# Kernel optimization log

Hardware: AMD Instinct MI355X
Metric: run time of the kernel (lower is better)

## Reference

```python
import jax, jax.numpy as jnp
import numpy as np

B, D, H = 8, 512, 8
HD = D // H            # 64 head dim
NS, NT = 8192, 4096    # search / template points
ATTN_EPS = 1e-6
LN_EPS = 1e-5


def layer_norm(x, g, b):
    m = jnp.mean(x, axis=-1, keepdims=True)
    v = jnp.mean((x - m) ** 2, axis=-1, keepdims=True)
    return (x - m) * jax.lax.rsqrt(v + LN_EPS) * g + b


def setup_inputs() -> dict:
    key = jax.random.key(0)
    ks = jax.random.split(key, 20)
    s = 0.02
    return {
        "search_feat": jax.random.normal(ks[0], (B, D, NS), jnp.float32),
        "search_xyz": jax.random.uniform(ks[1], (B, NS, 3), jnp.float32),
        "template_feat": jax.random.normal(ks[2], (B, D, NT), jnp.float32),
        "template_xyz": jax.random.uniform(ks[3], (B, NT, 3), jnp.float32),
        "pos_w1": jax.random.normal(ks[4], (3, D), jnp.float32) * s,
        "pos_b1": jnp.zeros((D,), jnp.float32),
        "pos_w2": jax.random.normal(ks[5], (D, D), jnp.float32) * s,
        "pos_b2": jnp.zeros((D,), jnp.float32),
        "wq": jax.random.normal(ks[6], (D, D), jnp.float32) * s,
        "wk": jax.random.normal(ks[7], (D, D), jnp.float32) * s,
        "wv": jax.random.normal(ks[8], (D, D), jnp.float32) * s,
        "w_merge": jax.random.normal(ks[9], (D, D), jnp.float32) * s,
        "mlp_w1": jax.random.normal(ks[10], (2 * D, 2 * D), jnp.float32) * s,
        "mlp_w2": jax.random.normal(ks[11], (2 * D, D), jnp.float32) * s,
        "ln1_g": jnp.ones((D,), jnp.float32),
        "ln1_b": jnp.zeros((D,), jnp.float32),
        "ln2_g": jnp.ones((D,), jnp.float32),
        "ln2_b": jnp.zeros((D,), jnp.float32),
    }


def reference(search_feat, search_xyz, template_feat, template_xyz,
              pos_w1, pos_b1, pos_w2, pos_b2, wq, wk, wv, w_merge,
              mlp_w1, mlp_w2, ln1_g, ln1_b, ln2_g, ln2_b):
    bs = search_feat.shape[0]
    sf = jnp.transpose(search_feat, (0, 2, 1))    # [B, Ns, D]
    tf = jnp.transpose(template_feat, (0, 2, 1))  # [B, Nt, D]

    # positional MLP on template coordinates
    pos = jax.nn.relu(template_xyz @ pos_w1 + pos_b1) @ pos_w2 + pos_b2
    tf_pos = tf + pos

    q = (sf @ wq).reshape(bs, NS, H, HD)
    k = (tf @ wk).reshape(bs, NT, H, HD)
    v = (tf_pos @ wv).reshape(bs, NT, H, HD)

    # LoFTR-style linear attention: phi(x) = elu(x) + 1
    Q = jax.nn.elu(q) + 1.0
    K = jax.nn.elu(k) + 1.0
    v_len = v.shape[1]
    v_n = v / v_len
    KV = jnp.einsum("bshd,bshv->bhdv", K, v_n)                 # [B,H,d,d]
    Z = 1.0 / (jnp.einsum("blhd,bhd->blh", Q, K.sum(axis=1)) + ATTN_EPS)
    msg = jnp.einsum("blhd,bhdv->blhv", Q, KV) * Z[..., None] * v_len

    msg = msg.reshape(bs, NS, H * HD) @ w_merge
    msg = layer_norm(msg, ln1_g, ln1_b)
    cat = jnp.concatenate([sf, msg], axis=2)                    # [B,Ns,2D]
    msg = jax.nn.relu(cat @ mlp_w1) @ mlp_w2
    msg = layer_norm(msg, ln2_g, ln2_b)
    return jnp.transpose(sf + msg, (0, 2, 1))                   # [B,D,Ns]
```

## Files before the change

kernel.cpp:

```cpp
#include <hip/hip_runtime.h>
#include <stdint.h>
#include <stddef.h>


using ushort_t = unsigned short;
using short8 = __attribute__((ext_vector_type(8))) short;
using f32x4  = __attribute__((ext_vector_type(4))) float;

#define DEVI __device__ __forceinline__

DEVI float b2f(unsigned short u) {
    unsigned v = ((unsigned)u) << 16;
    return __builtin_bit_cast(float, v);
}
DEVI unsigned short f2b(float x) {
    unsigned u = __builtin_bit_cast(unsigned, x);
    u += 0x7FFFu + ((u >> 16) & 1u);
    return (unsigned short)(u >> 16);
}
DEVI void gload16(const void* g, void* l) {
    __builtin_amdgcn_global_load_lds(
        (const __attribute__((address_space(1))) unsigned*)g,
        (__attribute__((address_space(3))) unsigned*)l, 16, 0, 0);
}

template <int EPI>
__global__ __launch_bounds__(512, 2)
void gemm_bf16(const ushort_t* __restrict__ A0, const ushort_t* __restrict__ A1,
               const ushort_t* __restrict__ Wt, ushort_t* __restrict__ C,
               const float* __restrict__ bias, const ushort_t* __restrict__ addm,
               int N, int K, int K0, int lda0, int lda1, int nn)
{
    __shared__ ushort_t As[2][256 * 64];
    __shared__ ushort_t Bs[2][256 * 64];
    const int tid = threadIdx.x;
    const int cpx = gridDim.x >> 3;
    const int lid = (blockIdx.x & 7) * cpx + (blockIdx.x >> 3);
    const int m0 = (lid / nn) * 256;
    const int n0 = (lid % nn) * 256;
    const int w = tid >> 6, l = tid & 63;
    const int wm = (w >> 2) * 128;
    const int wn = (w & 3) * 64;
    const int lr = l & 15, lg = l >> 4;
    const int srow = tid >> 3;
    const int sck  = (tid & 7) ^ (srow & 7);
    const int nk = K / 64;

    f32x4 acc[8][4] = {};

    auto stageA = [&](int kt, int buf) {
        const int kb = kt * 64;
        const ushort_t* p; int ld;
        if (kb < K0) { p = A0 + (size_t)m0 * lda0 + kb; ld = lda0; }
        else         { p = A1 + (size_t)m0 * lda1 + (kb - K0); ld = lda1; }
        p += (size_t)srow * ld + sck * 8;
#pragma unroll
        for (int j = 0; j < 4; j++)
            gload16(p + (size_t)(j * 64) * ld,
                    (void*)(&As[buf][j * 4096] + tid * 8));
    };
    auto stageB = [&](int kt, int buf) {
        const ushort_t* p = Wt + (size_t)(n0 + srow) * K + kt * 64 + sck * 8;
#pragma unroll
        for (int j = 0; j < 4; j++)
            gload16(p + (size_t)(j * 64) * K,
                    (void*)(&Bs[buf][j * 4096] + tid * 8));
    };

    stageA(0, 0); stageB(0, 0);
    asm volatile("s_waitcnt vmcnt(0)" ::: "memory");
    asm volatile("s_barrier" ::: "memory");

    for (int t = 0; t < nk; ++t) {
        const int cur = t & 1;
        const bool pre = (t + 1) < nk;
        short8 afr[4], bfr[4];

        auto ldA = [&](int mh, int ks) {
#pragma unroll
            for (int mf = 0; mf < 4; mf++) {
                const int r = wm + mh * 64 + mf * 16 + lr;
                afr[mf] = *(const short8*)&As[cur][r * 64 + ((ks * 4 + lg) ^ (r & 7)) * 8];
            }
        };
        auto ldB = [&](int ks) {
#pragma unroll
            for (int nf = 0; nf < 4; nf++) {
                const int r = wn + nf * 16 + lr;
                bfr[nf] = *(const short8*)&Bs[cur][r * 64 + ((ks * 4 + lg) ^ (r & 7)) * 8];
            }
        };
        auto mm = [&](int mh) {
            __builtin_amdgcn_s_setprio(1);
#pragma unroll
            for (int mf = 0; mf < 4; mf++)
#pragma unroll
                for (int nf = 0; nf < 4; nf++)
                    acc[mh * 4 + mf][nf] = __builtin_amdgcn_mfma_f32_16x16x32_bf16(
                        afr[mf], bfr[nf], acc[mh * 4 + mf][nf], 0, 0, 0);
            __builtin_amdgcn_s_setprio(0);
        };

        ldB(0); ldA(0, 0);
        if (pre) stageA(t + 1, cur ^ 1);
        asm volatile("s_barrier" ::: "memory");
        mm(0);
        asm volatile("s_barrier" ::: "memory");
        ldA(1, 0);
        if (pre) stageB(t + 1, cur ^ 1);
        asm volatile("s_barrier" ::: "memory");
        mm(1);
        asm volatile("s_barrier" ::: "memory");
        ldB(1); ldA(0, 1);
        asm volatile("s_barrier" ::: "memory");
        mm(0);
        asm volatile("s_barrier" ::: "memory");
        ldA(1, 1);
        asm volatile("s_waitcnt vmcnt(0)" ::: "memory");
        asm volatile("s_barrier" ::: "memory");
        mm(1);
        asm volatile("s_barrier" ::: "memory");
    }

#pragma unroll
    for (int mi = 0; mi < 8; mi++) {
        const int mh = mi >> 2, mf = mi & 3;
#pragma unroll
        for (int i = 0; i < 4; i++) {
            const int m = m0 + wm + mh * 64 + mf * 16 + lg * 4 + i;
#pragma unroll
            for (int nf = 0; nf < 4; nf++) {
                const int n = n0 + wn + nf * 16 + lr;
                float x = acc[mi][nf][i];
                if constexpr (EPI == 1) { x = x > 0.f ? x + 1.f : __expf(x); }
                if constexpr (EPI == 2) { x += bias[n] + b2f(addm[(size_t)m * N + n]); }
                if constexpr (EPI == 3) { x = fmaxf(x, 0.f); }
                C[(size_t)m * N + n] = f2b(x);
            }
        }
    }
}

__global__ __launch_bounds__(256)
void transpose_f32_bf16(const float* __restrict__ in, ushort_t* __restrict__ out,
                        int R, int Cc)
{
    __shared__ float tile[64][65];
    const int t = threadIdx.x;
    const int c0 = blockIdx.x * 64, r0 = blockIdx.y * 64;
    const size_t bo = (size_t)blockIdx.z * (size_t)R * (size_t)Cc;
    const float* src = in + bo;
    ushort_t* dst = out + bo;
#pragma unroll
    for (int i = 0; i < 4; i++) {
        const int r = (t >> 4) + i * 16;
        const int c = (t & 15) * 4;
        const float4 v = *(const float4*)&src[(size_t)(r0 + r) * Cc + c0 + c];
        tile[r][c + 0] = v.x; tile[r][c + 1] = v.y;
        tile[r][c + 2] = v.z; tile[r][c + 3] = v.w;
    }
    __syncthreads();
#pragma unroll
    for (int i = 0; i < 2; i++) {
        const int c = (t >> 3) + i * 32;
        const int rs = (t & 7) * 8;
        short8 o;
#pragma unroll
        for (int j = 0; j < 8; j++) o[j] = (short)f2b(tile[rs + j][c]);
        *(short8*)&dst[(size_t)(c0 + c) * R + r0 + rs] = o;
    }
}

__global__ __launch_bounds__(256)
void pos_mlp1(const float* __restrict__ xyz, const float* __restrict__ w1,
              const float* __restrict__ b1, ushort_t* __restrict__ P1)
{
    const int t = threadIdx.x;
    const int m = blockIdx.x * 4 + (t >> 6);
    const int n0 = (t & 63) * 8;
    const float x = xyz[m * 3 + 0], y = xyz[m * 3 + 1], z = xyz[m * 3 + 2];
    short8 o;
#pragma unroll
    for (int j = 0; j < 8; j++) {
        const int n = n0 + j;
        float v = x * w1[n] + y * w1[512 + n] + z * w1[1024 + n] + b1[n];
        o[j] = (short)f2b(fmaxf(v, 0.f));
    }
    *(short8*)&P1[(size_t)m * 512 + n0] = o;
}

__global__ __launch_bounds__(256)
void kv_partial(const ushort_t* __restrict__ Kp, const ushort_t* __restrict__ V,
                float* __restrict__ KVp, float* __restrict__ Ksp)
{
    __shared__ ushort_t Ks[256 * 64];
    __shared__ ushort_t Vs[256 * 64];
    const int t = threadIdx.x;
    const int sp = blockIdx.x, h = blockIdx.y, b = blockIdx.z;
    const int d0 = t >> 2, e0 = (t & 3) * 16;
    const int srow = t >> 3, scol = (t & 7) * 8;
    float acc[16] = {};
    float ksum = 0.f;
    for (int c = 0; c < 4; c++) {
        if (c) __syncthreads();
        const size_t sbase = (size_t)b * 4096 + sp * 1024 + c * 256;
#pragma unroll
        for (int i = 0; i < 8; i++) {
            const size_t go = (sbase + i * 32 + srow) * 512 + h * 64 + scol;
            gload16(Kp + go, (void*)(&Ks[i * 2048] + t * 8));
            gload16(V + go, (void*)(&Vs[i * 2048] + t * 8));
        }
        __syncthreads();
        for (int s = 0; s < 256; s++) {
            const float k = b2f(Ks[s * 64 + d0]);
            if ((t & 3) == 0) ksum += k;
            const short8 v0 = *(const short8*)&Vs[s * 64 + e0];
            const short8 v1 = *(const short8*)&Vs[s * 64 + e0 + 8];
#pragma unroll
            for (int j = 0; j < 8; j++) {
                acc[j]     += k * b2f((unsigned short)v0[j]);
                acc[8 + j] += k * b2f((unsigned short)v1[j]);
            }
        }
    }
    const int bh = b * 8 + h;
    float* kvo = KVp + (((size_t)sp * 64 + bh) * 64 + d0) * 64 + e0;
#pragma unroll
    for (int j = 0; j < 16; j++) kvo[j] = acc[j];
    if ((t & 3) == 0) Ksp[((size_t)sp * 64 + bh) * 64 + d0] = ksum;
}

__global__ __launch_bounds__(256)
void kv_finalize(const float* __restrict__ KVp, const float* __restrict__ Ksp,
                 ushort_t* __restrict__ KVt)
{
    const int bh = blockIdx.x, t = threadIdx.x;
    ushort_t* o = KVt + (size_t)bh * 5120;
#pragma unroll
    for (int i = 0; i < 16; i++) {
        const int idx = i * 256 + t;
        const int e = idx >> 6, d = idx & 63;
        float s = 0.f;
#pragma unroll
        for (int sp = 0; sp < 4; sp++)
            s += KVp[(((size_t)sp * 64 + bh) * 64 + d) * 64 + e];
        o[idx] = f2b(s);
    }
    if (t < 64) {
        float s = 0.f;
#pragma unroll
        for (int sp = 0; sp < 4; sp++) s += Ksp[((size_t)sp * 64 + bh) * 64 + t];
        o[4096 + t] = f2b(s);
    }
    for (int idx = 4160 + t; idx < 5120; idx += 256) o[idx] = 0;
}

__global__ __launch_bounds__(256, 2)
void attn_apply(const ushort_t* __restrict__ Qp, const ushort_t* __restrict__ KVt,
                ushort_t* __restrict__ msg1)
{
    __shared__ ushort_t As[256 * 64];
    __shared__ ushort_t Bs[80 * 64];
    const int t = threadIdx.x;
    const int ch = blockIdx.x, h = blockIdx.y, b = blockIdx.z;
    const int w = t >> 6, l = t & 63;
    const int lr = l & 15, lg = l >> 4;
    const int row0 = ch * 256;
    const int srow = t >> 3;
    const int sc = ((t & 7) ^ (srow & 7)) * 8;
    const ushort_t* kv = KVt + (size_t)(b * 8 + h) * 5120;
#pragma unroll
    for (int i = 0; i < 2; i++)
        gload16(kv + (size_t)(i * 32 + srow) * 64 + sc,
                (void*)(&Bs[i * 2048] + t * 8));
    if (t < 128)
        gload16(kv + (size_t)(64 + srow) * 64 + sc,
                (void*)(&Bs[4096] + t * 8));
    const ushort_t* qb = Qp + ((size_t)b * 8192 + row0) * 512 + h * 64;
#pragma unroll
    for (int i = 0; i < 8; i++)
        gload16(qb + (size_t)(i * 32 + srow) * 512 + sc,
                (void*)(&As[i * 2048] + t * 8));
    __syncthreads();
    f32x4 acc[4][5] = {};
    const int wr = w * 64;
#pragma unroll
    for (int ks = 0; ks < 2; ks++) {
        const int kswz = ((ks * 4 + lg) ^ (lr & 7)) * 8;
        short8 a[4], bb[5];
#pragma unroll
        for (int mf = 0; mf < 4; mf++)
            a[mf] = *(const short8*)&As[(wr + mf * 16 + lr) * 64 + kswz];
#pragma unroll
        for (int nf = 0; nf < 5; nf++)
            bb[nf] = *(const short8*)&Bs[(nf * 16 + lr) * 64 + kswz];
#pragma unroll
        for (int mf = 0; mf < 4; mf++)
#pragma unroll
            for (int nf = 0; nf < 5; nf++)
                acc[mf][nf] = __builtin_amdgcn_mfma_f32_16x16x32_bf16(
                    a[mf], bb[nf], acc[mf][nf], 0, 0, 0);
    }
#pragma unroll
    for (int mf = 0; mf < 4; mf++) {
#pragma unroll
        for (int i = 0; i < 4; i++) {
            const int m = row0 + wr + mf * 16 + lg * 4 + i;
            const float zden = __shfl(acc[mf][4][i], (l & 48));
            const float z = 1.f / (zden + 1e-6f);
#pragma unroll
            for (int nf = 0; nf < 4; nf++) {
                const int e = nf * 16 + lr;
                msg1[((size_t)b * 8192 + m) * 512 + h * 64 + e] =
                    f2b(acc[mf][nf][i] * z);
            }
        }
    }
}

__global__ __launch_bounds__(256)
void layer_norm_k(ushort_t* __restrict__ X, const float* __restrict__ g,
                  const float* __restrict__ bta)
{
    const int t = threadIdx.x;
    const int row = blockIdx.x * 4 + (t >> 6);
    const int l = t & 63;
    ushort_t* x = X + (size_t)row * 512;
    const short8 v = *(const short8*)&x[l * 8];
    float f[8];
    float s = 0.f;
#pragma unroll
    for (int j = 0; j < 8; j++) { f[j] = b2f((unsigned short)v[j]); s += f[j]; }
#pragma unroll
    for (int o = 32; o > 0; o >>= 1) s += __shfl_xor(s, o);
    const float mean = s * (1.f / 512.f);
    float vs = 0.f;
#pragma unroll
    for (int j = 0; j < 8; j++) { const float d = f[j] - mean; vs += d * d; }
#pragma unroll
    for (int o = 32; o > 0; o >>= 1) vs += __shfl_xor(vs, o);
    const float rstd = rsqrtf(vs * (1.f / 512.f) + 1e-5f);
    short8 ov;
#pragma unroll
    for (int j = 0; j < 8; j++) {
        const int c = l * 8 + j;
        ov[j] = (short)f2b((f[j] - mean) * rstd * g[c] + bta[c]);
    }
    *(short8*)&x[l * 8] = ov;
}

__global__ __launch_bounds__(256)
void ln2_final(const ushort_t* __restrict__ outp, const ushort_t* __restrict__ sfT,
               const float* __restrict__ g, const float* __restrict__ bta,
               float* __restrict__ out)
{
    __shared__ ushort_t tile[64][514];
    const int t = threadIdx.x;
    const int ns0 = blockIdx.x * 64, b = blockIdx.y;
    const int w = t >> 6, l = t & 63;
#pragma unroll
    for (int rr = 0; rr < 16; rr++) {
        const int r = w * 16 + rr;
        const size_t grow = (size_t)b * 8192 + ns0 + r;
        const short8 v = *(const short8*)&outp[grow * 512 + l * 8];
        float f[8];
        float s = 0.f;
#pragma unroll
        for (int j = 0; j < 8; j++) { f[j] = b2f((unsigned short)v[j]); s += f[j]; }
#pragma unroll
        for (int o = 32; o > 0; o >>= 1) s += __shfl_xor(s, o);
        const float mean = s * (1.f / 512.f);
        float vs = 0.f;
#pragma unroll
        for (int j = 0; j < 8; j++) { const float d = f[j] - mean; vs += d * d; }
#pragma unroll
        for (int o = 32; o > 0; o >>= 1) vs += __shfl_xor(vs, o);
        const float rstd = rsqrtf(vs * (1.f / 512.f) + 1e-5f);
        const short8 sv = *(const short8*)&sfT[grow * 512 + l * 8];
        short8 ov;
#pragma unroll
        for (int j = 0; j < 8; j++) {
            const int c = l * 8 + j;
            ov[j] = (short)f2b(b2f((unsigned short)sv[j]) +
                               (f[j] - mean) * rstd * g[c] + bta[c]);
        }
        *(short8*)&tile[r][l * 8] = ov;
    }
    __syncthreads();
#pragma unroll
    for (int i = 0; i < 32; i++) {
        const int d = (t >> 4) + i * 16;
        const int nss = (t & 15) * 4;
        float4 o;
        o.x = b2f(tile[nss + 0][d]);
        o.y = b2f(tile[nss + 1][d]);
        o.z = b2f(tile[nss + 2][d]);
        o.w = b2f(tile[nss + 3][d]);
        *(float4*)&out[((size_t)b * 512 + d) * 8192 + ns0 + nss] = o;
    }
}

extern "C" void kernel_launch(void* const* d_in, const int* in_sizes, int n_in,
                              void* d_out, int out_size, void* d_ws, size_t ws_size,
                              hipStream_t stream)
{
    (void)in_sizes; (void)n_in; (void)out_size; (void)ws_size;
    const float* search_feat   = (const float*)d_in[0];
    const float* template_feat = (const float*)d_in[2];
    const float* template_xyz  = (const float*)d_in[3];
    const float* pos_w1  = (const float*)d_in[4];
    const float* pos_b1  = (const float*)d_in[5];
    const float* pos_w2  = (const float*)d_in[6];
    const float* pos_b2  = (const float*)d_in[7];
    const float* wq      = (const float*)d_in[8];
    const float* wk      = (const float*)d_in[9];
    const float* wv      = (const float*)d_in[10];
    const float* w_merge = (const float*)d_in[11];
    const float* mlp_w1  = (const float*)d_in[12];
    const float* mlp_w2  = (const float*)d_in[13];
    const float* ln1_g   = (const float*)d_in[14];
    const float* ln1_b   = (const float*)d_in[15];
    const float* ln2_g   = (const float*)d_in[16];
    const float* ln2_b   = (const float*)d_in[17];
    float* out = (float*)d_out;

    char* ws = (char*)d_ws;
    ushort_t* sfT    = (ushort_t*)(ws + 0);
    ushort_t* Qp     = (ushort_t*)(ws + 67108864);
    ushort_t* tfT    = (ushort_t*)(ws + 134217728);
    ushort_t* Kp     = (ushort_t*)(ws + 167772160);
    ushort_t* msg2   = (ushort_t*)(ws + 134217728);
    ushort_t* P1     = (ushort_t*)(ws + 201326592);
    ushort_t* Vv     = (ushort_t*)(ws + 201326592);
    ushort_t* tfpos  = (ushort_t*)(ws + 234881024);
    ushort_t* msg1   = (ushort_t*)(ws + 268435456);
    ushort_t* hidden = (ushort_t*)(ws + 201326592);
    ushort_t* outp   = Qp;
    ushort_t* wqT  = (ushort_t*)(ws + 335544320);
    ushort_t* wkT  = (ushort_t*)(ws + 336068608);
    ushort_t* wvT  = (ushort_t*)(ws + 336592896);
    ushort_t* wmT  = (ushort_t*)(ws + 337117184);
    ushort_t* pw2T = (ushort_t*)(ws + 337641472);
    ushort_t* w1T  = (ushort_t*)(ws + 338165760);
    ushort_t* w2T  = (ushort_t*)(ws + 340262912);
    float*    KVp  = (float*)(ws + 341311488);
    float*    Ksp  = (float*)(ws + 345505792);
    ushort_t* KVt  = (ushort_t*)(ws + 345571328);

    transpose_f32_bf16<<<dim3(128, 8, 8), 256, 0, stream>>>(search_feat, sfT, 512, 8192);
    transpose_f32_bf16<<<dim3(64, 8, 8), 256, 0, stream>>>(template_feat, tfT, 512, 4096);
    transpose_f32_bf16<<<dim3(8, 8, 1), 256, 0, stream>>>(wq, wqT, 512, 512);
    transpose_f32_bf16<<<dim3(8, 8, 1), 256, 0, stream>>>(wk, wkT, 512, 512);
    transpose_f32_bf16<<<dim3(8, 8, 1), 256, 0, stream>>>(wv, wvT, 512, 512);
    transpose_f32_bf16<<<dim3(8, 8, 1), 256, 0, stream>>>(w_merge, wmT, 512, 512);
    transpose_f32_bf16<<<dim3(8, 8, 1), 256, 0, stream>>>(pos_w2, pw2T, 512, 512);
    transpose_f32_bf16<<<dim3(16, 16, 1), 256, 0, stream>>>(mlp_w1, w1T, 1024, 1024);
    transpose_f32_bf16<<<dim3(8, 16, 1), 256, 0, stream>>>(mlp_w2, w2T, 1024, 512);

    gemm_bf16<1><<<dim3(512), 512, 0, stream>>>(sfT, nullptr, wqT, Qp,
                                                nullptr, nullptr, 512, 512, 512, 512, 0, 2);
    gemm_bf16<1><<<dim3(256), 512, 0, stream>>>(tfT, nullptr, wkT, Kp,
                                                nullptr, nullptr, 512, 512, 512, 512, 0, 2);
    pos_mlp1<<<dim3(8192), 256, 0, stream>>>(template_xyz, pos_w1, pos_b1, P1);
    gemm_bf16<2><<<dim3(256), 512, 0, stream>>>(P1, nullptr, pw2T, tfpos,
                                                pos_b2, tfT, 512, 512, 512, 512, 0, 2);
    gemm_bf16<0><<<dim3(256), 512, 0, stream>>>(tfpos, nullptr, wvT, Vv,
                                                nullptr, nullptr, 512, 512, 512, 512, 0, 2);
    kv_partial<<<dim3(4, 8, 8), 256, 0, stream>>>(Kp, Vv, KVp, Ksp);
    kv_finalize<<<dim3(64), 256, 0, stream>>>(KVp, Ksp, KVt);
    attn_apply<<<dim3(32, 8, 8), 256, 0, stream>>>(Qp, KVt, msg1);
    gemm_bf16<0><<<dim3(512), 512, 0, stream>>>(msg1, nullptr, wmT, msg2,
                                                nullptr, nullptr, 512, 512, 512, 512, 0, 2);
    layer_norm_k<<<dim3(16384), 256, 0, stream>>>(msg2, ln1_g, ln1_b);
    gemm_bf16<3><<<dim3(1024), 512, 0, stream>>>(sfT, msg2, w1T, hidden,
                                                 nullptr, nullptr, 1024, 1024, 512, 512, 512, 4);
    gemm_bf16<0><<<dim3(512), 512, 0, stream>>>(hidden, nullptr, w2T, outp,
                                                nullptr, nullptr, 512, 1024, 1024, 1024, 0, 2);
    ln2_final<<<dim3(128, 8), 256, 0, stream>>>(outp, sfT, ln2_g, ln2_b, out);
}
```

Baseline: 741.3 us.

## Software-pipeline GEMM LDS fragment loads and cut per-iteration barriers to one

Reworks the bf16 MFMA GEMM main loop so LDS fragment reads are double-buffered in registers (aP/aQ/aR, b0/b1). Each fragment set is loaded one MFMA block ahead of its use, and the eight barriers per k-tile drop to a single barrier after the global prefetch completes. The accumulators are split into two 4x4 halves, and the epilogue is adjusted to match. The aim is to overlap LDS reads with MFMA work and remove synchronization stalls, at the cost of more live fragment registers and possible occupancy or spill pressure.

Result: faster. 707.1 us (-4.6%).

```diff
diff --git a/kernel.cpp b/kernel.cpp
--- a/kernel.cpp
+++ b/kernel.cpp
@@ -46,7 +46,8 @@
     const int sck  = (tid & 7) ^ (srow & 7);
     const int nk = K / 64;
 
-    f32x4 acc[8][4] = {};
+    f32x4 accA[4][4] = {};
+    f32x4 accB[4][4] = {};
 
     auto stageA = [&](int kt, int buf) {
         const int kb = kt * 64;
@@ -67,75 +68,79 @@
                     (void*)(&Bs[buf][j * 4096] + tid * 8));
     };
 
+    short8 aP[4], aQ[4], aR[4], b0[4], b1[4];
+
+    auto ldA = [&](short8 (&dst)[4], int mh, int ks, int cb) {
+#pragma unroll
+        for (int mf = 0; mf < 4; mf++) {
+            const int r = wm + mh * 64 + mf * 16 + lr;
+            dst[mf] = *(const short8*)&As[cb][r * 64 + ((ks * 4 + lg) ^ (r & 7)) * 8];
+        }
+    };
+    auto ldB = [&](short8 (&dst)[4], int ks, int cb) {
+#pragma unroll
+        for (int nf = 0; nf < 4; nf++) {
+            const int r = wn + nf * 16 + lr;
+            dst[nf] = *(const short8*)&Bs[cb][r * 64 + ((ks * 4 + lg) ^ (r & 7)) * 8];
+        }
+    };
+    auto MM = [&](f32x4 (&ac)[4][4], short8 (&af)[4], short8 (&bf)[4]) {
+        __builtin_amdgcn_s_setprio(1);
+#pragma unroll
+        for (int mf = 0; mf < 4; mf++)
+#pragma unroll
+            for (int nf = 0; nf < 4; nf++)
+                ac[mf][nf] = __builtin_amdgcn_mfma_f32_16x16x32_bf16(
+                    af[mf], bf[nf], ac[mf][nf], 0, 0, 0);
+        __builtin_amdgcn_s_setprio(0);
+    };
+
     stageA(0, 0); stageB(0, 0);
     asm volatile("s_waitcnt vmcnt(0)" ::: "memory");
-    asm volatile("s_barrier" ::: "memory");
+    __builtin_amdgcn_s_barrier();
+    ldA(aP, 0, 0, 0); ldB(b0, 0, 0);
 
     for (int t = 0; t < nk; ++t) {
         const int cur = t & 1;
         const bool pre = (t + 1) < nk;
-        short8 afr[4], bfr[4];
-
-        auto ldA = [&](int mh, int ks) {
-#pragma unroll
-            for (int mf = 0; mf < 4; mf++) {
-                const int r = wm + mh * 64 + mf * 16 + lr;
-                afr[mf] = *(const short8*)&As[cur][r * 64 + ((ks * 4 + lg) ^ (r & 7)) * 8];
-            }
-        };
-        auto ldB = [&](int ks) {
-#pragma unroll
-            for (int nf = 0; nf < 4; nf++) {
-                const int r = wn + nf * 16 + lr;
-                bfr[nf] = *(const short8*)&Bs[cur][r * 64 + ((ks * 4 + lg) ^ (r & 7)) * 8];
-            }
-        };
-        auto mm = [&](int mh) {
-            __builtin_amdgcn_s_setprio(1);
-#pragma unroll
-            for (int mf = 0; mf < 4; mf++)
-#pragma unroll
-                for (int nf = 0; nf < 4; nf++)
-                    acc[mh * 4 + mf][nf] = __builtin_amdgcn_mfma_f32_16x16x32_bf16(
-                        afr[mf], bfr[nf], acc[mh * 4 + mf][nf], 0, 0, 0);
-            __builtin_amdgcn_s_setprio(0);
-        };
-
-        ldB(0); ldA(0, 0);
+        ldA(aQ, 1, 0, cur); ldB(b1, 1, cur);
         if (pre) stageA(t + 1, cur ^ 1);
-        asm volatile("s_barrier" ::: "memory");
-        mm(0);
-        asm volatile("s_barrier" ::: "memory");
-        ldA(1, 0);
+        MM(accA, aP, b0);
+        ldA(aR, 0, 1, cur);
         if (pre) stageB(t + 1, cur ^ 1);
-        asm volatile("s_barrier" ::: "memory");
-        mm(1);
-        asm volatile("s_barrier" ::: "memory");
-        ldB(1); ldA(0, 1);
-        asm volatile("s_barrier" ::: "memory");
-        mm(0);
-        asm volatile("s_barrier" ::: "memory");
-        ldA(1, 1);
-        asm volatile("s_waitcnt vmcnt(0)" ::: "memory");
-        asm volatile("s_barrier" ::: "memory");
-        mm(1);
-        asm volatile("s_barrier" ::: "memory");
-    }
-
-#pragma unroll
-    for (int mi = 0; mi < 8; mi++) {
-        const int mh = mi >> 2, mf = mi & 3;
+        MM(accB, aQ, b0);
+        ldA(aP, 1, 1, cur);
+        MM(accA, aR, b1);
+        MM(accB, aP, b1);
+        if (pre) {
+            asm volatile("s_waitcnt vmcnt(0)" ::: "memory");
+            __builtin_amdgcn_s_barrier();
+            ldA(aP, 0, 0, cur ^ 1); ldB(b0, 0, cur ^ 1);
+        }
+    }
+
+#pragma unroll
+    for (int mf = 0; mf < 4; mf++) {
 #pragma unroll
         for (int i = 0; i < 4; i++) {
-            const int m = m0 + wm + mh * 64 + mf * 16 + lg * 4 + i;
+            const int mA = m0 + wm + mf * 16 + lg * 4 + i;
+            const int mB = mA + 64;
 #pragma unroll
             for (int nf = 0; nf < 4; nf++) {
                 const int n = n0 + wn + nf * 16 + lr;
-                float x = acc[mi][nf][i];
-                if constexpr (EPI == 1) { x = x > 0.f ? x + 1.f : __expf(x); }
-                if constexpr (EPI == 2) { x += bias[n] + b2f(addm[(size_t)m * N + n]); }
-                if constexpr (EPI == 3) { x = fmaxf(x, 0.f); }
-                C[(size_t)m * N + n] = f2b(x);
+                float x = accA[mf][nf][i];
+                float y = accB[mf][nf][i];
+                if constexpr (EPI == 1) {
+                    x = x > 0.f ? x + 1.f : __expf(x);
+                    y = y > 0.f ? y + 1.f : __expf(y);
+                }
+                if constexpr (EPI == 2) {
+                    x += bias[n] + b2f(addm[(size_t)mA * N + n]);
+                    y += bias[n] + b2f(addm[(size_t)mB * N + n]);
+                }
+                if constexpr (EPI == 3) { x = fmaxf(x, 0.f); y = fmaxf(y, 0.f); }
+                C[(size_t)mA * N + n] = f2b(x);
+                C[(size_t)mB * N + n] = f2b(y);
             }
         }
     }
```

## Restructure GEMM main loop into 4-buffer BK=32 pipeline with prefetch distance 2

Applied to the files above, without the earlier changes.

Replaces the double-buffered BK=64 GEMM loop, which had many intra-iteration barriers, with a 4-slot ring of BK=32 tiles. Loads run two stages ahead and each iteration ends with a single vmcnt wait and barrier. The LDS footprint is the same, and the swizzle is changed to suit 32-wide rows. The aim is to overlap global loads with MFMA and cut barrier count, at the cost of a shorter K step per barrier and possible new LDS bank conflicts from the narrower swizzle.

Result: slower. 825.4 us (+11.4%).

```diff
diff --git a/kernel.cpp b/kernel.cpp
--- a/kernel.cpp
+++ b/kernel.cpp
@@ -31,8 +31,8 @@
                const float* __restrict__ bias, const ushort_t* __restrict__ addm,
                int N, int K, int K0, int lda0, int lda1, int nn)
 {
-    __shared__ ushort_t As[2][256 * 64];
-    __shared__ ushort_t Bs[2][256 * 64];
+    __shared__ ushort_t As[4][256 * 32];
+    __shared__ ushort_t Bs[4][256 * 32];
     const int tid = threadIdx.x;
     const int cpx = gridDim.x >> 3;
     const int lid = (blockIdx.x & 7) * cpx + (blockIdx.x >> 3);
@@ -42,96 +42,77 @@
     const int wm = (w >> 2) * 128;
     const int wn = (w & 3) * 64;
     const int lr = l & 15, lg = l >> 4;
-    const int srow = tid >> 3;
-    const int sck  = (tid & 7) ^ (srow & 7);
-    const int nk = K / 64;
+    const int srow = tid >> 2;
+    const int sck  = (tid & 3) ^ ((srow >> 1) & 3);
+    const int nk = K / 32;
 
     f32x4 acc[8][4] = {};
 
     auto stageA = [&](int kt, int buf) {
-        const int kb = kt * 64;
+        const int kb = kt * 32;
         const ushort_t* p; int ld;
         if (kb < K0) { p = A0 + (size_t)m0 * lda0 + kb; ld = lda0; }
         else         { p = A1 + (size_t)m0 * lda1 + (kb - K0); ld = lda1; }
         p += (size_t)srow * ld + sck * 8;
 #pragma unroll
-        for (int j = 0; j < 4; j++)
-            gload16(p + (size_t)(j * 64) * ld,
+        for (int j = 0; j < 2; j++)
+            gload16(p + (size_t)(j * 128) * ld,
                     (void*)(&As[buf][j * 4096] + tid * 8));
     };
     auto stageB = [&](int kt, int buf) {
-        const ushort_t* p = Wt + (size_t)(n0 + srow) * K + kt * 64 + sck * 8;
-#pragma unroll
-        for (int j = 0; j < 4; j++)
-            gload16(p + (size_t)(j * 64) * K,
+        const ushort_t* p = Wt + (size_t)(n0 + srow) * K + kt * 32 + sck * 8;
+#pragma unroll
+        for (int j = 0; j < 2; j++)
+            gload16(p + (size_t)(j * 128) * K,
                     (void*)(&Bs[buf][j * 4096] + tid * 8));
     };
 
     stageA(0, 0); stageB(0, 0);
-    asm volatile("s_waitcnt vmcnt(0)" ::: "memory");
-    asm volatile("s_barrier" ::: "memory");
+    stageA(1, 1); stageB(1, 1);
+    asm volatile("s_waitcnt vmcnt(4)" ::: "memory");
+    __builtin_amdgcn_s_barrier();
 
     for (int t = 0; t < nk; ++t) {
-        const int cur = t & 1;
-        const bool pre = (t + 1) < nk;
-        short8 afr[4], bfr[4];
-
-        auto ldA = [&](int mh, int ks) {
-#pragma unroll
-            for (int mf = 0; mf < 4; mf++) {
-                const int r = wm + mh * 64 + mf * 16 + lr;
-                afr[mf] = *(const short8*)&As[cur][r * 64 + ((ks * 4 + lg) ^ (r & 7)) * 8];
-            }
-        };
-        auto ldB = [&](int ks) {
-#pragma unroll
-            for (int nf = 0; nf < 4; nf++) {
-                const int r = wn + nf * 16 + lr;
-                bfr[nf] = *(const short8*)&Bs[cur][r * 64 + ((ks * 4 + lg) ^ (r & 7)) * 8];
-            }
-        };
-        auto mm = [&](int mh) {
-            __builtin_amdgcn_s_setprio(1);
-#pragma unroll
-            for (int mf = 0; mf < 4; mf++)
-#pragma unroll
-                for (int nf = 0; nf < 4; nf++)
-                    acc[mh * 4 + mf][nf] = __builtin_amdgcn_mfma_f32_16x16x32_bf16(
-                        afr[mf], bfr[nf], acc[mh * 4 + mf][nf], 0, 0, 0);
-            __builtin_amdgcn_s_setprio(0);
-        };
-
-        ldB(0); ldA(0, 0);
-        if (pre) stageA(t + 1, cur ^ 1);
-        asm volatile("s_barrier" ::: "memory");
-        mm(0);
-        asm volatile("s_barrier" ::: "memory");
-        ldA(1, 0);
-        if (pre) stageB(t + 1, cur ^ 1);
-        asm volatile("s_barrier" ::: "memory");
-        mm(1);
-        asm volatile("s_barrier" ::: "memory");
-        ldB(1); ldA(0, 1);
-        asm volatile("s_barrier" ::: "memory");
-        mm(0);
-        asm volatile("s_barrier" ::: "memory");
-        ldA(1, 1);
-        asm volatile("s_waitcnt vmcnt(0)" ::: "memory");
-        asm volatile("s_barrier" ::: "memory");
-        mm(1);
-        asm volatile("s_barrier" ::: "memory");
-    }
-
-#pragma unroll
-    for (int mi = 0; mi < 8; mi++) {
-        const int mh = mi >> 2, mf = mi & 3;
+        const int cur = t & 3;
+        const bool pre = (t + 2) < nk;
+        if (pre) { stageA(t + 2, (t + 2) & 3); stageB(t + 2, (t + 2) & 3); }
+
+        short8 af[8], bf[4];
+#pragma unroll
+        for (int mf = 0; mf < 8; mf++) {
+            const int r = wm + mf * 16 + lr;
+            af[mf] = *(const short8*)&As[cur][r * 32 + (lg ^ ((r >> 1) & 3)) * 8];
+        }
+#pragma unroll
+        for (int nf = 0; nf < 4; nf++) {
+            const int r = wn + nf * 16 + lr;
+            bf[nf] = *(const short8*)&Bs[cur][r * 32 + (lg ^ ((r >> 1) & 3)) * 8];
+        }
+        __builtin_amdgcn_s_setprio(1);
+#pragma unroll
+        for (int mf = 0; mf < 8; mf++)
+#pragma unroll
+            for (int nf = 0; nf < 4; nf++)
+                acc[mf][nf] = __builtin_amdgcn_mfma_f32_16x16x32_bf16(
+                    af[mf], bf[nf], acc[mf][nf], 0, 0, 0);
+        __builtin_amdgcn_s_setprio(0);
+
+        if (t + 1 < nk) {
+            if (pre) { asm volatile("s_waitcnt vmcnt(4)" ::: "memory"); }
+            else     { asm volatile("s_waitcnt vmcnt(0)" ::: "memory"); }
+            __builtin_amdgcn_s_barrier();
+        }
+    }
+
+#pragma unroll
+    for (int mf = 0; mf < 8; mf++) {
 #pragma unroll
         for (int i = 0; i < 4; i++) {
-            const int m = m0 + wm + mh * 64 + mf * 16 + lg * 4 + i;
+            const int m = m0 + wm + mf * 16 + lg * 4 + i;
 #pragma unroll
             for (int nf = 0; nf < 4; nf++) {
                 const int n = n0 + wn + nf * 16 + lr;
-                float x = acc[mi][nf][i];
+                float x = acc[mf][nf][i];
                 if constexpr (EPI == 1) { x = x > 0.f ? x + 1.f : __expf(x); }
                 if constexpr (EPI == 2) { x += bias[n] + b2f(addm[(size_t)m * N + n]); }
                 if constexpr (EPI == 3) { x = fmaxf(x, 0.f); }
```
